# Kernel tuning notes

Measured on AMD Instinct MI355X. Metric: run time of the kernel, lower is better.

The kernel has to match this reference:

```python
import jax, jax.numpy as jnp
import numpy as np

N_HEADS = 16
D_MODEL = 1024
D_K = D_MODEL // N_HEADS


def setup_inputs() -> dict:
    key = jax.random.key(0)
    ks = jax.random.split(key, 7)
    b, n = 4, 2048
    s = 0.02  # keep projections well-scaled
    return {
        "Q": jax.random.normal(ks[0], (b, n, D_MODEL), jnp.float32),
        "K": jax.random.normal(ks[1], (b, n, D_MODEL), jnp.float32),
        "V": jax.random.normal(ks[2], (b, n, D_MODEL), jnp.float32),
        "w_q": jax.random.normal(ks[3], (D_MODEL, D_MODEL), jnp.float32) * s,
        "w_k": jax.random.normal(ks[4], (D_MODEL, D_MODEL), jnp.float32) * s,
        "w_v": jax.random.normal(ks[5], (D_MODEL, D_MODEL), jnp.float32) * s,
        "w_o": jax.random.normal(ks[6], (D_MODEL, D_MODEL), jnp.float32) * s,
    }


def reference(Q, K, V, w_q, w_k, w_v, w_o):
    b, n, _ = Q.shape
    # nn.Linear(x) = x @ W.T ; weights stored [out, in]
    q = (Q @ w_q.T).reshape(b, n, N_HEADS, D_K).transpose(0, 2, 1, 3)  # [b,h,n,dk]
    k = (K @ w_k.T).reshape(b, n, N_HEADS, D_K).transpose(0, 2, 1, 3)
    v = (V @ w_v.T).reshape(b, n, N_HEADS, D_K).transpose(0, 2, 1, 3)
    scores = jnp.einsum("bhqd,bhkd->bhqk", q, k) / jnp.sqrt(jnp.float32(D_K))
    causal = jnp.tril(jnp.ones((n, n), dtype=bool))  # keep lower triangle incl. diag
    scores = jnp.where(causal[None, None], scores, -jnp.inf)
    weights = jax.nn.softmax(scores, axis=-1)
    attn = jnp.einsum("bhqk,bhkd->bhqd", weights, v)
    attn = attn.transpose(0, 2, 1, 3).reshape(b, n, D_MODEL)
    return attn @ w_o.T
```

## Files before the change

### kernel.cpp

```cpp
#include <hip/hip_runtime.h>
#include <hip/hip_bf16.h>
#include <cstdint>
#include <cstddef>


typedef __bf16 bf16_t;
typedef bf16_t bf16x4 __attribute__((ext_vector_type(4)));
typedef bf16_t bf16x8 __attribute__((ext_vector_type(8)));
typedef float floatx4 __attribute__((ext_vector_type(4)));

#define MFMA(a, b, c) __builtin_amdgcn_mfma_f32_16x16x32_bf16((a), (b), (c), 0, 0, 0)
#define NEG_BIG (-30000.0f)

static __device__ __forceinline__ bf16_t f2bf(float x) { return (bf16_t)x; }

static __device__ __forceinline__ bf16x8 cvt8p(const floatx4 a, const floatx4 b) {
  bf16x8 r;
  r[0] = (bf16_t)a[0]; r[1] = (bf16_t)a[1]; r[2] = (bf16_t)a[2]; r[3] = (bf16_t)a[3];
  r[4] = (bf16_t)b[0]; r[5] = (bf16_t)b[1]; r[6] = (bf16_t)b[2]; r[7] = (bf16_t)b[3];
  return r;
}

static __device__ __forceinline__ void g2l16(const void* g, void* l) {
  __builtin_amdgcn_global_load_lds(
      (const __attribute__((address_space(1))) void*)g,
      (__attribute__((address_space(3))) void*)l, 16, 0, 0);
}

__global__ void detect_dtype(const unsigned short* __restrict__ w,
                             int* __restrict__ flag) {
  const unsigned short u = w[threadIdx.x];
  const bool big = (u & 0x7F80u) >= 0x3F80u;
  const unsigned long long m = __ballot(big);
  if (threadIdx.x == 0) *flag = (m != 0ull) ? 1 : 0;
}

__global__ __launch_bounds__(256)
void cvt_bf16(const void* __restrict__ src, bf16_t* __restrict__ dst,
              int n8, const int* __restrict__ flag)
{
  const int i = blockIdx.x * 256 + threadIdx.x;
  if (i >= n8) return;
  if (*flag) {
    const floatx4* s = (const floatx4*)src;
    ((bf16x8*)dst)[i] = cvt8p(s[2 * i], s[2 * i + 1]);
  } else {
    ((bf16x8*)dst)[i] = ((const bf16x8*)src)[i];
  }
}

static __device__ __forceinline__ void gemm_tile_map(int& bm, int& bn) {
  const int f  = (int)(blockIdx.y * gridDim.x + blockIdx.x);
  const int xj = f & 7, sq = f >> 3;
  bm = ((xj << 3) | (sq >> 3)) * 128;
  bn = (sq & 7) * 128;
}

template <typename OutT>
__global__ __launch_bounds__(256, 2)
void gemm_lds2(const bf16_t* __restrict__ A, const bf16_t* __restrict__ W,
               OutT* __restrict__ C)
{
  const int K = 1024;
  __shared__ __align__(16) bf16_t sA[2][128 * 32];
  __shared__ __align__(16) bf16_t sB[2][128 * 32];
  const int tid  = threadIdx.x;
  const int wave = tid >> 6;
  const int lane = tid & 63;
  const int wm = wave >> 1, wn = wave & 1;
  int bm, bn;
  gemm_tile_map(bm, bn);
  const int quad = lane >> 4, r16 = lane & 15;

  floatx4 acc[4][4];
  #pragma unroll
  for (int i = 0; i < 4; ++i)
    #pragma unroll
    for (int j = 0; j < 4; ++j) acc[i][j] = {0.f, 0.f, 0.f, 0.f};

  const int ch0 = wave * 2;
  const int r0  = lane >> 2;
  const int ce  = (lane & 3) * 8;
  const bf16_t* Ag0 = A + (size_t)(bm + ch0 * 16 + r0) * K + ce;
  const bf16_t* Ag1 = Ag0 + (size_t)16 * K;
  const bf16_t* Wg0 = W + (size_t)(bn + ch0 * 16 + r0) * K + ce;
  const bf16_t* Wg1 = Wg0 + (size_t)16 * K;

  auto stage = [&](int k0, int b) {
    g2l16(Ag0 + k0, &sA[b][ch0 * 512]);
    g2l16(Ag1 + k0, &sA[b][(ch0 + 1) * 512]);
    g2l16(Wg0 + k0, &sB[b][ch0 * 512]);
    g2l16(Wg1 + k0, &sB[b][(ch0 + 1) * 512]);
  };

  stage(0, 0);
  for (int t = 0; t < 32; ++t) {
    const int buf = t & 1;
    __syncthreads();
    if (t + 1 < 32) stage((t + 1) * 32, buf ^ 1);

    bf16x8 af[4], bv[4];
    #pragma unroll
    for (int mi = 0; mi < 4; ++mi)
      af[mi] = *(const bf16x8*)&sA[buf][(wm * 64 + mi * 16 + r16) * 32 + quad * 8];
    #pragma unroll
    for (int ni = 0; ni < 4; ++ni)
      bv[ni] = *(const bf16x8*)&sB[buf][(wn * 64 + ni * 16 + r16) * 32 + quad * 8];
    #pragma unroll
    for (int mi = 0; mi < 4; ++mi)
      #pragma unroll
      for (int ni = 0; ni < 4; ++ni)
        acc[mi][ni] = MFMA(af[mi], bv[ni], acc[mi][ni]);
  }

  #pragma unroll
  for (int mi = 0; mi < 4; ++mi)
    #pragma unroll
    for (int ni = 0; ni < 4; ++ni)
      #pragma unroll
      for (int r = 0; r < 4; ++r) {
        const int row = bm + wm * 64 + mi * 16 + quad * 4 + r;
        const int col = bn + wn * 64 + ni * 16 + r16;
        C[(size_t)row * 1024 + col] = (OutT)acc[mi][ni][r];
      }
}

template <bool WF32>
static __device__ __forceinline__
void gemm_hyb_core(const bf16_t* __restrict__ A, const void* __restrict__ Wv,
                   bf16_t* __restrict__ C,
                   bf16_t (*sA)[128 * 32], bf16_t (*sB)[128 * 40])
{
  const int K = 1024;
  const int tid  = threadIdx.x;
  const int wave = tid >> 6;
  const int lane = tid & 63;
  const int wm = wave >> 1, wn = wave & 1;
  int bm, bn;
  gemm_tile_map(bm, bn);
  const int quad = lane >> 4, r16 = lane & 15;

  floatx4 acc[4][4];
  #pragma unroll
  for (int i = 0; i < 4; ++i)
    #pragma unroll
    for (int j = 0; j < 4; ++j) acc[i][j] = {0.f, 0.f, 0.f, 0.f};

  const int ch0 = wave * 2;
  const int r0  = lane >> 2;
  const int ce  = (lane & 3) * 8;
  const bf16_t* Ag0 = A + (size_t)(bm + ch0 * 16 + r0) * K + ce;
  const bf16_t* Ag1 = Ag0 + (size_t)16 * K;

  const int srow = tid >> 2;
  const int scol = (tid & 3) * 8;
  const size_t w0 = (size_t)(bn + srow) * K + scol;
  const size_t w1 = w0 + (size_t)64 * K;

  floatx4 fw[2][2];
  bf16x8  bw[2];
  auto stageW = [&](int k0) {
    if constexpr (WF32) {
      const float* Wf = (const float*)Wv;
      fw[0][0] = *(const floatx4*)(Wf + w0 + k0);
      fw[0][1] = *(const floatx4*)(Wf + w0 + k0 + 4);
      fw[1][0] = *(const floatx4*)(Wf + w1 + k0);
      fw[1][1] = *(const floatx4*)(Wf + w1 + k0 + 4);
    } else {
      const bf16_t* Wb = (const bf16_t*)Wv;
      bw[0] = *(const bf16x8*)(Wb + w0 + k0);
      bw[1] = *(const bf16x8*)(Wb + w1 + k0);
    }
  };

  stageW(0);
  g2l16(Ag0, &sA[0][ch0 * 512]);
  g2l16(Ag1, &sA[0][(ch0 + 1) * 512]);

  for (int t = 0; t < 32; ++t) {
    const int buf = t & 1;
    {
      bf16x8 vb0, vb1;
      if constexpr (WF32) { vb0 = cvt8p(fw[0][0], fw[0][1]); vb1 = cvt8p(fw[1][0], fw[1][1]); }
      else                { vb0 = bw[0]; vb1 = bw[1]; }
      *(bf16x8*)&sB[buf][srow * 40 + scol]        = vb0;
      *(bf16x8*)&sB[buf][(srow + 64) * 40 + scol] = vb1;
    }
    __syncthreads();
    if (t + 1 < 32) {
      const int k0 = (t + 1) * 32;
      g2l16(Ag0 + k0, &sA[buf ^ 1][ch0 * 512]);
      g2l16(Ag1 + k0, &sA[buf ^ 1][(ch0 + 1) * 512]);
      stageW(k0);
    }

    bf16x8 af[4], bv[4];
    #pragma unroll
    for (int mi = 0; mi < 4; ++mi)
      af[mi] = *(const bf16x8*)&sA[buf][(wm * 64 + mi * 16 + r16) * 32 + quad * 8];
    #pragma unroll
    for (int ni = 0; ni < 4; ++ni)
      bv[ni] = *(const bf16x8*)&sB[buf][(wn * 64 + ni * 16 + r16) * 40 + quad * 8];
    #pragma unroll
    for (int mi = 0; mi < 4; ++mi)
      #pragma unroll
      for (int ni = 0; ni < 4; ++ni)
        acc[mi][ni] = MFMA(af[mi], bv[ni], acc[mi][ni]);
  }

  #pragma unroll
  for (int mi = 0; mi < 4; ++mi)
    #pragma unroll
    for (int ni = 0; ni < 4; ++ni)
      #pragma unroll
      for (int r = 0; r < 4; ++r) {
        const int row = bm + wm * 64 + mi * 16 + quad * 4 + r;
        const int col = bn + wn * 64 + ni * 16 + r16;
        C[(size_t)row * 1024 + col] = (bf16_t)acc[mi][ni][r];
      }
}

__global__ __launch_bounds__(256, 2)
void gemm_hyb(const bf16_t* __restrict__ A, const void* __restrict__ Wv,
              bf16_t* __restrict__ C, const int* __restrict__ flag)
{
  __shared__ __align__(16) bf16_t sA[2][128 * 32];
  __shared__ __align__(16) bf16_t sB[2][128 * 40];
  if (*flag) gemm_hyb_core<true >(A, Wv, C, sA, sB);
  else       gemm_hyb_core<false>(A, Wv, C, sA, sB);
}

__global__ __launch_bounds__(256, 4)
void flash_attn(bf16_t* qio, const bf16_t* __restrict__ kh,
                const bf16_t* __restrict__ vh)
{
  __shared__ __align__(16) bf16_t sK[64 * 64];
  __shared__ __align__(16) bf16_t sVt[64 * 64];
  __shared__ __align__(16) bf16_t sP[64 * 64];
  const int tid  = threadIdx.x;
  const int wave = tid >> 6;
  const int lane = tid & 63;
  const int quad = lane >> 4, r16 = lane & 15;

  const int f  = (int)(blockIdx.y * gridDim.x + blockIdx.x);
  const int xj = f & 7, sq = f >> 3;
  const int bh = xj + (sq >> 5) * 8;
  const int q0 = (31 - (sq & 31)) * 64;
  const int b = bh >> 4, h = bh & 15;
  const size_t hb = ((size_t)b * 2048) * 1024 + (size_t)h * 64;
  const int swl = (r16 & 7) << 3;

  bf16x8 qf[2];
  #pragma unroll
  for (int ks = 0; ks < 2; ++ks)
    qf[ks] = *(const bf16x8*)(qio + hb +
        (size_t)(q0 + wave * 16 + r16) * 1024 + ks * 32 + quad * 8);

  floatx4 o[4];
  #pragma unroll
  for (int nd = 0; nd < 4; ++nd) o[nd] = {0.f, 0.f, 0.f, 0.f};
  float mrow = NEG_BIG, lrow = 0.f;

  const float sc = 0.125f * 1.44269504089f;
  const int kend = q0 + 64;
  const int qrow = q0 + wave * 16 + r16;

  bf16x8 kst[2], vst[2];
  #pragma unroll
  for (int j = 0; j < 2; ++j) {
    const int c = j * 256 + tid;
    kst[j] = *(const bf16x8*)(kh + hb + (size_t)(c >> 3) * 1024 + (c & 7) * 8);
    vst[j] = *(const bf16x8*)(vh + hb + (size_t)(c & 63) * 1024 + (c >> 6) * 8);
  }

  for (int kv0 = 0; kv0 < kend; kv0 += 64) {
    #pragma unroll
    for (int j = 0; j < 2; ++j) {
      const int c = j * 256 + tid;
      const int krow = c >> 3, kcol = (c & 7) * 8;
      *(bf16x8*)&sK[krow * 64 + (kcol ^ ((krow & 7) << 3))] = kst[j];
      const int vkv = c & 63, vd = (c >> 6) * 8;
      #pragma unroll
      for (int e = 0; e < 8; ++e)
        sVt[(vd + e) * 64 + (vkv ^ (e << 3))] = vst[j][e];
    }
    __syncthreads();

    if (kv0 + 64 < kend) {
      #pragma unroll
      for (int j = 0; j < 2; ++j) {
        const int c = j * 256 + tid;
        kst[j] = *(const bf16x8*)(kh + hb + (size_t)(kv0 + 64 + (c >> 3)) * 1024 + (c & 7) * 8);
        vst[j] = *(const bf16x8*)(vh + hb + (size_t)(kv0 + 64 + (c & 63)) * 1024 + (c >> 6) * 8);
      }
    }

    floatx4 st[4];
    #pragma unroll
    for (int nk = 0; nk < 4; ++nk) st[nk] = {0.f, 0.f, 0.f, 0.f};
    #pragma unroll
    for (int ks = 0; ks < 2; ++ks) {
      bf16x8 bk[4];
      #pragma unroll
      for (int nk = 0; nk < 4; ++nk)
        bk[nk] = *(const bf16x8*)&sK[(nk * 16 + r16) * 64 + ((ks * 32 + quad * 8) ^ swl)];
      #pragma unroll
      for (int nk = 0; nk < 4; ++nk)
        st[nk] = MFMA(bk[nk], qf[ks], st[nk]);
    }

    const bool domask = (kv0 + 63 > q0 + wave * 16);
    #pragma unroll
    for (int nk = 0; nk < 4; ++nk)
      #pragma unroll
      for (int r = 0; r < 4; ++r) {
        float t = st[nk][r] * sc;
        if (domask && (kv0 + nk * 16 + quad * 4 + r > qrow)) t = NEG_BIG;
        st[nk][r] = t;
      }

    float mx = fmaxf(fmaxf(st[0][0], st[0][1]), fmaxf(st[0][2], st[0][3]));
    #pragma unroll
    for (int nk = 1; nk < 4; ++nk)
      mx = fmaxf(mx, fmaxf(fmaxf(st[nk][0], st[nk][1]),
                           fmaxf(st[nk][2], st[nk][3])));
    mx = fmaxf(mx, __shfl_xor(mx, 16, 64));
    mx = fmaxf(mx, __shfl_xor(mx, 32, 64));

    if (!__all(mx <= mrow)) {
      const float mnew  = fmaxf(mrow, mx);
      const float alpha = exp2f(mrow - mnew);
      mrow = mnew;
      lrow *= alpha;
      #pragma unroll
      for (int r = 0; r < 4; ++r) {
        const float ar = __shfl(alpha, quad * 4 + r, 64);
        #pragma unroll
        for (int nd = 0; nd < 4; ++nd) o[nd][r] *= ar;
      }
    }

    float ls = 0.f;
    #pragma unroll
    for (int nk = 0; nk < 4; ++nk) {
      bf16x4 pk;
      #pragma unroll
      for (int r = 0; r < 4; ++r) {
        const bf16_t pb = f2bf(exp2f(st[nk][r] - mrow));
        ls += (float)pb;
        pk[r] = pb;
      }
      *(bf16x4*)&sP[(wave * 16 + r16) * 64 + ((nk * 16 + quad * 4) ^ swl)] = pk;
    }
    ls += __shfl_xor(ls, 16, 64);
    ls += __shfl_xor(ls, 32, 64);
    lrow += ls;
    __syncthreads();

    #pragma unroll
    for (int ks = 0; ks < 2; ++ks) {
      const int cb = (ks * 32 + quad * 8) ^ swl;
      const bf16x8 pa = *(const bf16x8*)&sP[(wave * 16 + r16) * 64 + cb];
      bf16x8 vb[4];
      #pragma unroll
      for (int nd = 0; nd < 4; ++nd)
        vb[nd] = *(const bf16x8*)&sVt[(nd * 16 + r16) * 64 + cb];
      #pragma unroll
      for (int nd = 0; nd < 4; ++nd)
        o[nd] = MFMA(pa, vb[nd], o[nd]);
    }
    __syncthreads();
  }

  #pragma unroll
  for (int r = 0; r < 4; ++r) {
    const float lr  = __shfl(lrow, quad * 4 + r, 64);
    const float inv = 1.f / lr;
    const int row = q0 + wave * 16 + quad * 4 + r;
    #pragma unroll
    for (int nd = 0; nd < 4; ++nd)
      qio[hb + (size_t)row * 1024 + nd * 16 + r16] = f2bf(o[nd][r] * inv);
  }
}

extern "C" void kernel_launch(void* const* d_in, const int* in_sizes, int n_in,
                              void* d_out, int out_size, void* d_ws, size_t ws_size,
                              hipStream_t stream) {
  (void)in_sizes; (void)n_in; (void)out_size; (void)ws_size;
  const size_t TSZ = (size_t)8192 * 1024;
  const size_t WSZ = (size_t)1024 * 1024;
  int*    flag = (int*)d_ws;
  bf16_t* qws  = (bf16_t*)((char*)d_ws + 16);
  bf16_t* kws  = qws + TSZ;
  bf16_t* vws  = (bf16_t*)d_out;
  bf16_t* abuf = (bf16_t*)d_out + TSZ;

  const int nA8 = (int)(TSZ / 8);
  const int nW8 = (int)(WSZ / 8);

  detect_dtype<<<1, 64, 0, stream>>>((const unsigned short*)d_in[3], flag);

  const dim3 gg(8, 64);

  cvt_bf16<<<nA8 / 256, 256, 0, stream>>>(d_in[2], abuf, nA8, flag);
  cvt_bf16<<<nW8 / 256, 256, 0, stream>>>(d_in[5], kws, nW8, flag);
  gemm_lds2<bf16_t><<<gg, 256, 0, stream>>>(abuf, kws, vws);

  cvt_bf16<<<nA8 / 256, 256, 0, stream>>>(d_in[0], abuf, nA8, flag);
  cvt_bf16<<<nW8 / 256, 256, 0, stream>>>(d_in[3], kws, nW8, flag);
  gemm_lds2<bf16_t><<<gg, 256, 0, stream>>>(abuf, kws, qws);

  cvt_bf16<<<nA8 / 256, 256, 0, stream>>>(d_in[1], abuf, nA8, flag);
  gemm_hyb<<<gg, 256, 0, stream>>>(abuf, d_in[4], kws, flag);

  flash_attn<<<dim3(64, 32), 256, 0, stream>>>(qws, kws, vws);

  cvt_bf16<<<nW8 / 256, 256, 0, stream>>>(d_in[6], kws, nW8, flag);
  gemm_lds2<float><<<gg, 256, 0, stream>>>(qws, kws, (float*)d_out);
}
```

Baseline: 420.2 us.

## Fuse fp32 activation conversion into batched QKV GEMM with swizzled weight layout

Removes the separate full-tensor bf16 conversion passes over the Q/K/V activations. The GEMM now loads fp32 activations into registers, converts them and writes them to padded LDS, while the weights are pre-converted into an XOR-swizzled layout and streamed in with global_load_lds. The three projections run as one launch via a z grid dimension, and occupancy is raised to 3 blocks per CU. This trades extra register-path load work and LDS padding for far less global memory traffic and fewer kernel launches.

```diff
diff --git a/kernel.cpp b/kernel.cpp
--- a/kernel.cpp
+++ b/kernel.cpp
@@ -36,17 +36,24 @@
 }
 
 __global__ __launch_bounds__(256)
-void cvt_bf16(const void* __restrict__ src, bf16_t* __restrict__ dst,
-              int n8, const int* __restrict__ flag)
+void cvt_w_swz(const void* __restrict__ s0, const void* __restrict__ s1,
+               const void* __restrict__ s2, bf16_t* __restrict__ dst,
+               const int* __restrict__ flag)
 {
-  const int i = blockIdx.x * 256 + threadIdx.x;
-  if (i >= n8) return;
+  const void* src = blockIdx.y == 0 ? s0 : (blockIdx.y == 1 ? s1 : s2);
+  bf16_t* d = dst + (size_t)blockIdx.y * (1024 * 1024);
+  const int i    = blockIdx.x * 256 + threadIdx.x;
+  const int row  = i >> 7;
+  const int col0 = (i & 127) * 8;
+  const int dcol = col0 ^ ((row & 6) << 2);
+  bf16x8 v;
   if (*flag) {
-    const floatx4* s = (const floatx4*)src;
-    ((bf16x8*)dst)[i] = cvt8p(s[2 * i], s[2 * i + 1]);
+    const float* s = (const float*)src + (size_t)row * 1024 + col0;
+    v = cvt8p(*(const floatx4*)s, *(const floatx4*)(s + 4));
   } else {
-    ((bf16x8*)dst)[i] = ((const bf16x8*)src)[i];
-  }
+    v = *(const bf16x8*)((const bf16_t*)src + (size_t)row * 1024 + col0);
+  }
+  *(bf16x8*)(d + (size_t)row * 1024 + dcol) = v;
 }
 
 static __device__ __forceinline__ void gemm_tile_map(int& bm, int& bn) {
@@ -56,80 +63,11 @@
   bn = (sq & 7) * 128;
 }
 
-template <typename OutT>
-__global__ __launch_bounds__(256, 2)
-void gemm_lds2(const bf16_t* __restrict__ A, const bf16_t* __restrict__ W,
-               OutT* __restrict__ C)
-{
-  const int K = 1024;
-  __shared__ __align__(16) bf16_t sA[2][128 * 32];
-  __shared__ __align__(16) bf16_t sB[2][128 * 32];
-  const int tid  = threadIdx.x;
-  const int wave = tid >> 6;
-  const int lane = tid & 63;
-  const int wm = wave >> 1, wn = wave & 1;
-  int bm, bn;
-  gemm_tile_map(bm, bn);
-  const int quad = lane >> 4, r16 = lane & 15;
-
-  floatx4 acc[4][4];
-  #pragma unroll
-  for (int i = 0; i < 4; ++i)
-    #pragma unroll
-    for (int j = 0; j < 4; ++j) acc[i][j] = {0.f, 0.f, 0.f, 0.f};
-
-  const int ch0 = wave * 2;
-  const int r0  = lane >> 2;
-  const int ce  = (lane & 3) * 8;
-  const bf16_t* Ag0 = A + (size_t)(bm + ch0 * 16 + r0) * K + ce;
-  const bf16_t* Ag1 = Ag0 + (size_t)16 * K;
-  const bf16_t* Wg0 = W + (size_t)(bn + ch0 * 16 + r0) * K + ce;
-  const bf16_t* Wg1 = Wg0 + (size_t)16 * K;
-
-  auto stage = [&](int k0, int b) {
-    g2l16(Ag0 + k0, &sA[b][ch0 * 512]);
-    g2l16(Ag1 + k0, &sA[b][(ch0 + 1) * 512]);
-    g2l16(Wg0 + k0, &sB[b][ch0 * 512]);
-    g2l16(Wg1 + k0, &sB[b][(ch0 + 1) * 512]);
-  };
-
-  stage(0, 0);
-  for (int t = 0; t < 32; ++t) {
-    const int buf = t & 1;
-    __syncthreads();
-    if (t + 1 < 32) stage((t + 1) * 32, buf ^ 1);
-
-    bf16x8 af[4], bv[4];
-    #pragma unroll
-    for (int mi = 0; mi < 4; ++mi)
-      af[mi] = *(const bf16x8*)&sA[buf][(wm * 64 + mi * 16 + r16) * 32 + quad * 8];
-    #pragma unroll
-    for (int ni = 0; ni < 4; ++ni)
-      bv[ni] = *(const bf16x8*)&sB[buf][(wn * 64 + ni * 16 + r16) * 32 + quad * 8];
-    #pragma unroll
-    for (int mi = 0; mi < 4; ++mi)
-      #pragma unroll
-      for (int ni = 0; ni < 4; ++ni)
-        acc[mi][ni] = MFMA(af[mi], bv[ni], acc[mi][ni]);
-  }
-
-  #pragma unroll
-  for (int mi = 0; mi < 4; ++mi)
-    #pragma unroll
-    for (int ni = 0; ni < 4; ++ni)
-      #pragma unroll
-      for (int r = 0; r < 4; ++r) {
-        const int row = bm + wm * 64 + mi * 16 + quad * 4 + r;
-        const int col = bn + wn * 64 + ni * 16 + r16;
-        C[(size_t)row * 1024 + col] = (OutT)acc[mi][ni][r];
-      }
-}
-
-template <bool WF32>
+template <bool AF32, typename OutT>
 static __device__ __forceinline__
-void gemm_hyb_core(const bf16_t* __restrict__ A, const void* __restrict__ Wv,
-                   bf16_t* __restrict__ C,
-                   bf16_t (*sA)[128 * 32], bf16_t (*sB)[128 * 40])
+void gemm_rs_core(const void* __restrict__ Av, const bf16_t* __restrict__ W,
+                  OutT* __restrict__ C,
+                  bf16_t (*sA)[128 * 40], bf16_t (*sB)[128 * 32])
 {
   const int K = 1024;
   const int tid  = threadIdx.x;
@@ -139,68 +77,69 @@
   int bm, bn;
   gemm_tile_map(bm, bn);
   const int quad = lane >> 4, r16 = lane & 15;
+  const int cW = (quad * 8) ^ ((r16 & 6) << 2);
 
   floatx4 acc[4][4];
   #pragma unroll
   for (int i = 0; i < 4; ++i)
     #pragma unroll
     for (int j = 0; j < 4; ++j) acc[i][j] = {0.f, 0.f, 0.f, 0.f};
+
+  const int srow = tid >> 2;
+  const int scol = (tid & 3) * 8;
+  const size_t a0 = (size_t)(bm + srow) * K + scol;
+  const size_t a1 = a0 + (size_t)64 * K;
 
   const int ch0 = wave * 2;
   const int r0  = lane >> 2;
   const int ce  = (lane & 3) * 8;
-  const bf16_t* Ag0 = A + (size_t)(bm + ch0 * 16 + r0) * K + ce;
-  const bf16_t* Ag1 = Ag0 + (size_t)16 * K;
-
-  const int srow = tid >> 2;
-  const int scol = (tid & 3) * 8;
-  const size_t w0 = (size_t)(bn + srow) * K + scol;
-  const size_t w1 = w0 + (size_t)64 * K;
-
-  floatx4 fw[2][2];
-  bf16x8  bw[2];
-  auto stageW = [&](int k0) {
-    if constexpr (WF32) {
-      const float* Wf = (const float*)Wv;
-      fw[0][0] = *(const floatx4*)(Wf + w0 + k0);
-      fw[0][1] = *(const floatx4*)(Wf + w0 + k0 + 4);
-      fw[1][0] = *(const floatx4*)(Wf + w1 + k0);
-      fw[1][1] = *(const floatx4*)(Wf + w1 + k0 + 4);
+  const bf16_t* Wg0 = W + (size_t)(bn + ch0 * 16 + r0) * K + ce;
+  const bf16_t* Wg1 = Wg0 + (size_t)16 * K;
+
+  floatx4 fa[2][2];
+  bf16x8  ba[2];
+  auto stageA = [&](int k0) {
+    if constexpr (AF32) {
+      const float* Af = (const float*)Av;
+      fa[0][0] = *(const floatx4*)(Af + a0 + k0);
+      fa[0][1] = *(const floatx4*)(Af + a0 + k0 + 4);
+      fa[1][0] = *(const floatx4*)(Af + a1 + k0);
+      fa[1][1] = *(const floatx4*)(Af + a1 + k0 + 4);
     } else {
-      const bf16_t* Wb = (const bf16_t*)Wv;
-      bw[0] = *(const bf16x8*)(Wb + w0 + k0);
-      bw[1] = *(const bf16x8*)(Wb + w1 + k0);
+      const bf16_t* Ab = (const bf16_t*)Av;
+      ba[0] = *(const bf16x8*)(Ab + a0 + k0);
+      ba[1] = *(const bf16x8*)(Ab + a1 + k0);
     }
   };
 
-  stageW(0);
-  g2l16(Ag0, &sA[0][ch0 * 512]);
-  g2l16(Ag1, &sA[0][(ch0 + 1) * 512]);
+  stageA(0);
+  g2l16(Wg0, &sB[0][ch0 * 512]);
+  g2l16(Wg1, &sB[0][(ch0 + 1) * 512]);
 
   for (int t = 0; t < 32; ++t) {
     const int buf = t & 1;
     {
-      bf16x8 vb0, vb1;
-      if constexpr (WF32) { vb0 = cvt8p(fw[0][0], fw[0][1]); vb1 = cvt8p(fw[1][0], fw[1][1]); }
-      else                { vb0 = bw[0]; vb1 = bw[1]; }
-      *(bf16x8*)&sB[buf][srow * 40 + scol]        = vb0;
-      *(bf16x8*)&sB[buf][(srow + 64) * 40 + scol] = vb1;
+      bf16x8 va0, va1;
+      if constexpr (AF32) { va0 = cvt8p(fa[0][0], fa[0][1]); va1 = cvt8p(fa[1][0], fa[1][1]); }
+      else                { va0 = ba[0]; va1 = ba[1]; }
+      *(bf16x8*)&sA[buf][srow * 40 + scol]        = va0;
+      *(bf16x8*)&sA[buf][(srow + 64) * 40 + scol] = va1;
     }
     __syncthreads();
     if (t + 1 < 32) {
       const int k0 = (t + 1) * 32;
-      g2l16(Ag0 + k0, &sA[buf ^ 1][ch0 * 512]);
-      g2l16(Ag1 + k0, &sA[buf ^ 1][(ch0 + 1) * 512]);
-      stageW(k0);
+      g2l16(Wg0 + k0, &sB[buf ^ 1][ch0 * 512]);
+      g2l16(Wg1 + k0, &sB[buf ^ 1][(ch0 + 1) * 512]);
+      stageA(k0);
     }
 
     bf16x8 af[4], bv[4];
     #pragma unroll
     for (int mi = 0; mi < 4; ++mi)
-      af[mi] = *(const bf16x8*)&sA[buf][(wm * 64 + mi * 16 + r16) * 32 + quad * 8];
+      af[mi] = *(const bf16x8*)&sA[buf][(wm * 64 + mi * 16 + r16) * 40 + quad * 8];
     #pragma unroll
     for (int ni = 0; ni < 4; ++ni)
-      bv[ni] = *(const bf16x8*)&sB[buf][(wn * 64 + ni * 16 + r16) * 40 + quad * 8];
+      bv[ni] = *(const bf16x8*)&sB[buf][(wn * 64 + ni * 16 + r16) * 32 + cW];
     #pragma unroll
     for (int mi = 0; mi < 4; ++mi)
       #pragma unroll
@@ -216,18 +155,25 @@
       for (int r = 0; r < 4; ++r) {
         const int row = bm + wm * 64 + mi * 16 + quad * 4 + r;
         const int col = bn + wn * 64 + ni * 16 + r16;
-        C[(size_t)row * 1024 + col] = (bf16_t)acc[mi][ni][r];
-      }
-}
-
-__global__ __launch_bounds__(256, 2)
-void gemm_hyb(const bf16_t* __restrict__ A, const void* __restrict__ Wv,
-              bf16_t* __restrict__ C, const int* __restrict__ flag)
+        C[(size_t)row * 1024 + col] = (OutT)acc[mi][ni][r];
+      }
+}
+
+template <int ADT, typename OutT>
+__global__ __launch_bounds__(256, 3)
+void gemm_rs(const void* __restrict__ A0, const void* __restrict__ A1,
+             const void* __restrict__ A2, const bf16_t* __restrict__ Wb,
+             OutT* __restrict__ C0, OutT* __restrict__ C1,
+             OutT* __restrict__ C2, const int* __restrict__ flag)
 {
-  __shared__ __align__(16) bf16_t sA[2][128 * 32];
-  __shared__ __align__(16) bf16_t sB[2][128 * 40];
-  if (*flag) gemm_hyb_core<true >(A, Wv, C, sA, sB);
-  else       gemm_hyb_core<false>(A, Wv, C, sA, sB);
+  __shared__ __align__(16) bf16_t sA[2][128 * 40];
+  __shared__ __align__(16) bf16_t sB[2][128 * 32];
+  const int z = blockIdx.z;
+  const void*   A = z == 0 ? A0 : (z == 1 ? A1 : A2);
+  const bf16_t* W = Wb + (size_t)z * (1024 * 1024);
+  OutT*         C = z == 0 ? C0 : (z == 1 ? C1 : C2);
+  if (ADT == 0 && *flag) gemm_rs_core<true,  OutT>(A, W, C, sA, sB);
+  else                   gemm_rs_core<false, OutT>(A, W, C, sA, sB);
 }
 
 __global__ __launch_bounds__(256, 4)
@@ -388,33 +334,23 @@
                               hipStream_t stream) {
   (void)in_sizes; (void)n_in; (void)out_size; (void)ws_size;
   const size_t TSZ = (size_t)8192 * 1024;
-  const size_t WSZ = (size_t)1024 * 1024;
   int*    flag = (int*)d_ws;
   bf16_t* qws  = (bf16_t*)((char*)d_ws + 16);
   bf16_t* kws  = qws + TSZ;
   bf16_t* vws  = (bf16_t*)d_out;
-  bf16_t* abuf = (bf16_t*)d_out + TSZ;
-
-  const int nA8 = (int)(TSZ / 8);
-  const int nW8 = (int)(WSZ / 8);
+  bf16_t* wsl  = (bf16_t*)d_out + TSZ;
 
   detect_dtype<<<1, 64, 0, stream>>>((const unsigned short*)d_in[3], flag);
 
-  const dim3 gg(8, 64);
-
-  cvt_bf16<<<nA8 / 256, 256, 0, stream>>>(d_in[2], abuf, nA8, flag);
-  cvt_bf16<<<nW8 / 256, 256, 0, stream>>>(d_in[5], kws, nW8, flag);
-  gemm_lds2<bf16_t><<<gg, 256, 0, stream>>>(abuf, kws, vws);
-
-  cvt_bf16<<<nA8 / 256, 256, 0, stream>>>(d_in[0], abuf, nA8, flag);
-  cvt_bf16<<<nW8 / 256, 256, 0, stream>>>(d_in[3], kws, nW8, flag);
-  gemm_lds2<bf16_t><<<gg, 256, 0, stream>>>(abuf, kws, qws);
-
-  cvt_bf16<<<nA8 / 256, 256, 0, stream>>>(d_in[1], abuf, nA8, flag);
-  gemm_hyb<<<gg, 256, 0, stream>>>(abuf, d_in[4], kws, flag);
+  cvt_w_swz<<<dim3(512, 3), 256, 0, stream>>>(d_in[3], d_in[4], d_in[5], wsl, flag);
+
+  gemm_rs<0, bf16_t><<<dim3(8, 64, 3), 256, 0, stream>>>(
+      d_in[0], d_in[1], d_in[2], wsl, qws, kws, vws, flag);
 
   flash_attn<<<dim3(64, 32), 256, 0, stream>>>(qws, kws, vws);
 
-  cvt_bf16<<<nW8 / 256, 256, 0, stream>>>(d_in[6], kws, nW8, flag);
-  gemm_lds2<float><<<gg, 256, 0, stream>>>(qws, kws, (float*)d_out);
-}
+  cvt_w_swz<<<dim3(512, 1), 256, 0, stream>>>(d_in[6], d_in[6], d_in[6], kws, flag);
+
+  gemm_rs<1, float><<<dim3(8, 64, 1), 256, 0, stream>>>(
+      qws, qws, qws, kws, (float*)d_out, (float*)d_out, (float*)d_out, flag);
+}
```

New measurement: 402.3 us. -4.3%, faster.
